# Performance work log

Measured on AMD Instinct MI355X. Metric: run time of the kernel, lower is better.

## Reference

```python
import jax, jax.numpy as jnp
import numpy as np

B, S, D, H = 2, 2048, 2048, 16
DK = D // H
EPS = 1e-5


def _layernorm(x, g, b):
    m = jnp.mean(x, axis=-1, keepdims=True)
    v = jnp.mean(jnp.square(x - m), axis=-1, keepdims=True)
    return (x - m) * jax.lax.rsqrt(v + EPS) * g + b


def setup_inputs() -> dict:
    key = jax.random.key(0)
    ks = jax.random.split(key, 12)
    w = lambda k, shape: jax.random.normal(k, shape, jnp.float32) * 0.02
    return {
        "src": jax.random.normal(ks[0], (B, S, D), jnp.float32),
        "src_mask": jnp.tril(jnp.ones((S, S), jnp.float32))[None, None],  # [1,1,S,S] causal
        "Wq": w(ks[1], (D, D)), "bq": jnp.zeros((D,), jnp.float32),
        "Wk": w(ks[2], (D, D)), "bk": jnp.zeros((D,), jnp.float32),
        "Wv": w(ks[3], (D, D)), "bv": jnp.zeros((D,), jnp.float32),
        "Wo": w(ks[4], (D, D)), "bo": jnp.zeros((D,), jnp.float32),
        "ln1_g": jnp.ones((D,), jnp.float32), "ln1_b": jnp.zeros((D,), jnp.float32),
        "ln2_g": jnp.ones((D,), jnp.float32), "ln2_b": jnp.zeros((D,), jnp.float32),
        "W1": w(ks[5], (D, 4 * D)), "b1": jnp.zeros((4 * D,), jnp.float32),
        "W2": w(ks[6], (4 * D, D)), "b2": jnp.zeros((D,), jnp.float32),
    }


def reference(src, src_mask, Wq, bq, Wk, bk, Wv, bv, Wo, bo,
              ln1_g, ln1_b, ln2_g, ln2_b, W1, b1, W2, b2):
    b, s, d = src.shape
    dk = d // H
    # --- pre-LN attention ---
    x = _layernorm(src, ln1_g, ln1_b)
    q = (x @ Wq + bq).reshape(b, s, H, dk).transpose(0, 2, 1, 3)  # [b,h,s,dk]
    k = (x @ Wk + bk).reshape(b, s, H, dk).transpose(0, 2, 1, 3)
    v = (x @ Wv + bv).reshape(b, s, H, dk).transpose(0, 2, 1, 3)
    scores = jnp.einsum('bhqd,bhkd->bhqk', q, k) / np.sqrt(dk).astype(np.float32)
    scores = jnp.where(src_mask > 0, scores, jnp.float32(-1e9))
    attn = jax.nn.softmax(scores, axis=-1)
    ctx = jnp.einsum('bhqk,bhkd->bhqd', attn, v)
    ctx = ctx.transpose(0, 2, 1, 3).reshape(b, s, d)
    x = src + (ctx @ Wo + bo)  # residual (dropout is identity at eval)
    # --- pre-LN MLP ---
    y = _layernorm(x, ln2_g, ln2_b)
    y = jax.nn.gelu(y @ W1 + b1, approximate=False) @ W2 + b2
    return x + y
```

## Files before the change

kernel.cpp:

```cpp
#include <hip/hip_runtime.h>
#include <hip/hip_bf16.h>
#include <math.h>

#define DEV __device__ __forceinline__

typedef __attribute__((ext_vector_type(8))) short short8;
typedef __attribute__((ext_vector_type(4))) float f32x4;

template<bool B> struct BoolC { static constexpr bool value = B; };

DEV short f2bf(float f) {
  union { float f; unsigned u; } v; v.f = f;
  unsigned r = v.u + 0x7fffu + ((v.u >> 16) & 1u);
  return (short)(r >> 16);
}

DEV void gload16(const void* g, void* l) {
  __builtin_amdgcn_global_load_lds(
      (__attribute__((address_space(1))) void*)g,
      (__attribute__((address_space(3))) void*)l, 16, 0, 0);
}

DEV void bar() {
  asm volatile("" ::: "memory");
  __builtin_amdgcn_s_barrier();
  asm volatile("" ::: "memory");
}
template<int N> DEV void vwait() {
  if constexpr (N == 0)      asm volatile("s_waitcnt vmcnt(0)" ::: "memory");
  else if constexpr (N == 3) asm volatile("s_waitcnt vmcnt(3)" ::: "memory");
  else                       asm volatile("s_waitcnt vmcnt(4)" ::: "memory");
}

__global__ __launch_bounds__(256) void ln_kernel(
    const float* __restrict__ x, const float* __restrict__ g,
    const float* __restrict__ b, short* __restrict__ out) {
  int row = blockIdx.x;
  const float* xr = x + (size_t)row * 2048;
  int tid = threadIdx.x;
  float4 a0 = ((const float4*)xr)[tid * 2];
  float4 a1 = ((const float4*)xr)[tid * 2 + 1];
  float s = a0.x + a0.y + a0.z + a0.w + a1.x + a1.y + a1.z + a1.w;
  float q = a0.x*a0.x + a0.y*a0.y + a0.z*a0.z + a0.w*a0.w
          + a1.x*a1.x + a1.y*a1.y + a1.z*a1.z + a1.w*a1.w;
#pragma unroll
  for (int off = 32; off; off >>= 1) { s += __shfl_xor(s, off); q += __shfl_xor(q, off); }
  __shared__ float red[8];
  int w = tid >> 6;
  if ((tid & 63) == 0) { red[w] = s; red[4 + w] = q; }
  __syncthreads();
  s = red[0] + red[1] + red[2] + red[3];
  q = red[4] + red[5] + red[6] + red[7];
  float mean = s * (1.0f / 2048.0f);
  float var  = q * (1.0f / 2048.0f) - mean * mean;
  float rstd = rsqrtf(var + 1e-5f);
  float xv[8] = {a0.x, a0.y, a0.z, a0.w, a1.x, a1.y, a1.z, a1.w};
  short8 o;
#pragma unroll
  for (int j = 0; j < 8; ++j) {
    int col = tid * 8 + j;
    o[j] = f2bf((xv[j] - mean) * rstd * g[col] + b[col]);
  }
  *(short8*)(out + (size_t)row * 2048 + tid * 8) = o;
}

__global__ __launch_bounds__(256) void wt_kernel(
    const float* __restrict__ W, short* __restrict__ Wt, int K, int N) {
  __shared__ short tile[64][65];
  int k0 = blockIdx.x * 64, n0 = blockIdx.y * 64;
  int tx = threadIdx.x, ty = threadIdx.y;
#pragma unroll
  for (int r = 0; r < 16; ++r) {
    int kl = ty + r * 4;
    tile[kl][tx] = f2bf(W[(size_t)(k0 + kl) * N + n0 + tx]);
  }
  __syncthreads();
#pragma unroll
  for (int r = 0; r < 16; ++r) {
    int nl = ty + r * 4;
    Wt[(size_t)(n0 + nl) * K + k0 + tx] = tile[tx][nl];
  }
}

template <int BM, int EPI>
__global__ __launch_bounds__(512, 2) void gemm8_kernel(
    const short* __restrict__ A, const short* __restrict__ Bt, int K, int N,
    const float* __restrict__ bp1, const float* __restrict__ bp2,
    const float* __restrict__ bp3, const float* __restrict__ res,
    short* __restrict__ outb, float* __restrict__ outf, short* __restrict__ vt) {
  constexpr int MF  = BM / 32;
  constexpr int MG  = MF / 2;
  constexpr int SA  = BM * 64;
  constexpr int SB  = 16384;
  constexpr int CPA = BM / 128;
  constexpr int CPB = 2;
  constexpr int NW  = CPA + CPB;
  __shared__ char lds[4 * SA + 4 * SB];
  char* Ab = lds;
  char* Bb = lds + 4 * SA;
  int tid = threadIdx.x, lane = tid & 63, w = tid >> 6;
  int wm = w >> 2, wn = w & 3, hi = lane >> 4, lo = lane & 15;
  int bm = blockIdx.y * BM, bn = blockIdx.x * 256;

  const char* gA[CPA]; int lA[CPA];
  const char* gB[CPB]; int lB[CPB];
#pragma unroll
  for (int i = 0; i < CPA; ++i) {
    int c = w * CPA + i, r = c * 16 + (lane >> 2);
    gA[i] = (const char*)(A + (size_t)(bm + r) * K) + (((lane & 3) ^ ((r >> 1) & 3)) << 4);
    lA[i] = c * 1024;
  }
#pragma unroll
  for (int i = 0; i < CPB; ++i) {
    int c = w * CPB + i, r = c * 16 + (lane >> 2);
    gB[i] = (const char*)(Bt + (size_t)(bn + r) * K) + (((lane & 3) ^ ((r >> 1) & 3)) << 4);
    lB[i] = c * 1024;
  }
  auto stA = [&](int g) {
    char* d = Ab + (g & 3) * SA;
#pragma unroll
    for (int i = 0; i < CPA; ++i) gload16(gA[i] + (size_t)g * 64, d + lA[i]);
  };
  auto stB = [&](int g) {
    char* d = Bb + (g & 3) * SB;
#pragma unroll
    for (int i = 0; i < CPB; ++i) gload16(gB[i] + (size_t)g * 64, d + lB[i]);
  };

  int offA[MF], offB[4];
#pragma unroll
  for (int m = 0; m < MF; ++m) {
    int r = wm * (BM / 2) + m * 16 + lo;
    offA[m] = r * 64 + ((hi ^ ((r >> 1) & 3)) << 4);
  }
#pragma unroll
  for (int n = 0; n < 4; ++n) {
    int r = wn * 64 + n * 16 + lo;
    offB[n] = r * 64 + ((hi ^ ((r >> 1) & 3)) << 4);
  }

  f32x4 acc[MF][4];
#pragma unroll
  for (int m = 0; m < MF; ++m)
#pragma unroll
    for (int n = 0; n < 4; ++n) acc[m][n] = (f32x4){0.f, 0.f, 0.f, 0.f};

  stA(0); stB(0); stA(1); stB(1);
  vwait<NW>(); bar();

  int NT = K >> 6;
  auto tile = [&](int t, auto stc) {
    constexpr bool ST = decltype(stc)::value;
    char* sa0 = Ab + ((2 * t) & 3) * SA;     char* sb0 = Bb + ((2 * t) & 3) * SB;
    char* sa1 = Ab + ((2 * t + 1) & 3) * SA; char* sb1 = Bb + ((2 * t + 1) & 3) * SB;
    short8 bf[4], af[MG];
#pragma unroll
    for (int n = 0; n < 4; ++n) bf[n] = *(const short8*)(sb0 + offB[n]);
#pragma unroll
    for (int m = 0; m < MG; ++m) af[m] = *(const short8*)(sa0 + offA[m]);
    if constexpr (ST) stA(2 * t + 2);
    bar(); __builtin_amdgcn_s_setprio(1);
#pragma unroll
    for (int m = 0; m < MG; ++m)
#pragma unroll
      for (int n = 0; n < 4; ++n)
        acc[m][n] = __builtin_amdgcn_mfma_f32_16x16x32_bf16(af[m], bf[n], acc[m][n], 0, 0, 0);
    __builtin_amdgcn_s_setprio(0); bar();
#pragma unroll
    for (int m = 0; m < MG; ++m) af[m] = *(const short8*)(sa0 + offA[MG + m]);
    if constexpr (ST) stB(2 * t + 2);
    bar(); __builtin_amdgcn_s_setprio(1);
#pragma unroll
    for (int m = 0; m < MG; ++m)
#pragma unroll
      for (int n = 0; n < 4; ++n)
        acc[MG + m][n] = __builtin_amdgcn_mfma_f32_16x16x32_bf16(af[m], bf[n], acc[MG + m][n], 0, 0, 0);
    __builtin_amdgcn_s_setprio(0);
    if constexpr (ST) vwait<NW>(); else vwait<0>();
    bar();
#pragma unroll
    for (int n = 0; n < 4; ++n) bf[n] = *(const short8*)(sb1 + offB[n]);
#pragma unroll
    for (int m = 0; m < MG; ++m) af[m] = *(const short8*)(sa1 + offA[m]);
    if constexpr (ST) stA(2 * t + 3);
    bar(); __builtin_amdgcn_s_setprio(1);
#pragma unroll
    for (int m = 0; m < MG; ++m)
#pragma unroll
      for (int n = 0; n < 4; ++n)
        acc[m][n] = __builtin_amdgcn_mfma_f32_16x16x32_bf16(af[m], bf[n], acc[m][n], 0, 0, 0);
    __builtin_amdgcn_s_setprio(0); bar();
#pragma unroll
    for (int m = 0; m < MG; ++m) af[m] = *(const short8*)(sa1 + offA[MG + m]);
    if constexpr (ST) stB(2 * t + 3);
    bar(); __builtin_amdgcn_s_setprio(1);
#pragma unroll
    for (int m = 0; m < MG; ++m)
#pragma unroll
      for (int n = 0; n < 4; ++n)
        acc[MG + m][n] = __builtin_amdgcn_mfma_f32_16x16x32_bf16(af[m], bf[n], acc[MG + m][n], 0, 0, 0);
    __builtin_amdgcn_s_setprio(0);
    if constexpr (ST) vwait<NW>();
    bar();
  };

  for (int t = 0; t < NT - 1; ++t) tile(t, BoolC<true>{});
  tile(NT - 1, BoolC<false>{});

#pragma unroll
  for (int mf = 0; mf < MF; ++mf) {
#pragma unroll
    for (int nf = 0; nf < 4; ++nf) {
      int n = bn + wn * 64 + nf * 16 + lo;
#pragma unroll
      for (int r = 0; r < 4; ++r) {
        int m = bm + wm * (BM / 2) + mf * 16 + hi * 4 + r;
        float v = acc[mf][nf][r];
        if (EPI == 0) {
          float bb = (n < 2048) ? bp1[n] : (n < 4096) ? bp2[n - 2048] : bp3[n - 4096];
          v += bb;
          if (n < 2048) v *= 0.08838834764831845f;
          outb[(size_t)m * N + n] = f2bf(v);
          if (n >= 4096) {
            int b_ = m >> 11, s_ = m & 2047, h_ = (n - 4096) >> 7, dk = (n - 4096) & 127;
            vt[((size_t)((b_ * 16 + h_) * 128 + dk) << 11) + s_] = f2bf(v);
          }
        } else if (EPI == 1) {
          outf[(size_t)m * N + n] = res[(size_t)m * N + n] + v + bp1[n];
        } else {
          float t = v + bp1[n];
          outb[(size_t)m * N + n] = f2bf(0.5f * t * (1.0f + erff(t * 0.70710678118654752f)));
        }
      }
    }
  }
}

__global__ __launch_bounds__(256) void attn_kernel(
    const short* __restrict__ qkv, const short* __restrict__ vtb,
    short* __restrict__ ctx) {
  __shared__ char Kl[16384];
  __shared__ char Vl[16384];
  __shared__ char Pl[16384];
  int qt = blockIdx.x, bh = blockIdx.y;
  int b = bh >> 4, h = bh & 15;
  int tid = threadIdx.x, lane = tid & 63, w = tid >> 6;
  int hi = lane >> 4, lo = lane & 15;

  short8 qf[2][4];
#pragma unroll
  for (int mi = 0; mi < 2; ++mi)
#pragma unroll
    for (int ks = 0; ks < 4; ++ks) {
      int row = b * 2048 + qt * 128 + w * 32 + mi * 16 + lo;
      int col = h * 128 + ks * 32 + hi * 8;
      qf[mi][ks] = *(const short8*)(qkv + (size_t)row * 6144 + col);
    }

  f32x4 ao[2][8] = {};
  float mst[2][4], lst[2][4];
#pragma unroll
  for (int i = 0; i < 2; ++i)
#pragma unroll
    for (int r = 0; r < 4; ++r) { mst[i][r] = -1e30f; lst[i][r] = 0.f; }

  int nt = 2 * qt + 2;
  for (int t = 0; t < nt; ++t) {
    __syncthreads();
#pragma unroll
    for (int i = 0; i < 4; ++i) {
      int c = w * 4 + i;
      int kr = c * 4 + (lane >> 4);
      int dk16 = lo ^ (kr & 7);
      const short* kg = qkv + (size_t)(b * 2048 + t * 64 + kr) * 6144
                            + 2048 + h * 128 + dk16 * 8;
      gload16(kg, Kl + c * 1024);
      int vr = c * 8 + (lane >> 3);
      int kv16 = (lane & 7) ^ (vr & 7);
      const short* vg = vtb + (size_t)(bh * 128 + vr) * 2048 + t * 64 + kv16 * 8;
      gload16(vg, Vl + c * 1024);
    }
    __syncthreads();

    f32x4 sc[2][4] = {};
#pragma unroll
    for (int ks = 0; ks < 4; ++ks) {
      short8 kf[4];
#pragma unroll
      for (int ni = 0; ni < 4; ++ni) {
        int r = ni * 16 + lo;
        kf[ni] = *(const short8*)(Kl + r * 256 + (((ks * 4 + hi) ^ (r & 7)) << 4));
      }
#pragma unroll
      for (int mi = 0; mi < 2; ++mi)
#pragma unroll
        for (int ni = 0; ni < 4; ++ni)
          sc[mi][ni] = __builtin_amdgcn_mfma_f32_16x16x32_bf16(qf[mi][ks], kf[ni], sc[mi][ni], 0, 0, 0);
    }

    if (t >= 2 * qt) {
#pragma unroll
      for (int mi = 0; mi < 2; ++mi)
#pragma unroll
        for (int ni = 0; ni < 4; ++ni)
#pragma unroll
          for (int r = 0; r < 4; ++r) {
            int qrow = qt * 128 + w * 32 + mi * 16 + hi * 4 + r;
            int kv = t * 64 + ni * 16 + lo;
            if (kv > qrow) sc[mi][ni][r] = -1e9f;
          }
    }

#pragma unroll
    for (int mi = 0; mi < 2; ++mi)
#pragma unroll
      for (int r = 0; r < 4; ++r) {
        float vm = fmaxf(fmaxf(sc[mi][0][r], sc[mi][1][r]),
                         fmaxf(sc[mi][2][r], sc[mi][3][r]));
#pragma unroll
        for (int off = 8; off; off >>= 1) vm = fmaxf(vm, __shfl_xor(vm, off));
        float mn = fmaxf(mst[mi][r], vm);
        float corr = __expf(mst[mi][r] - mn);
        float ps = 0.f;
#pragma unroll
        for (int ni = 0; ni < 4; ++ni) {
          float p = __expf(sc[mi][ni][r] - mn);
          sc[mi][ni][r] = p; ps += p;
        }
#pragma unroll
        for (int off = 8; off; off >>= 1) ps += __shfl_xor(ps, off);
        lst[mi][r] = lst[mi][r] * corr + ps;
        mst[mi][r] = mn;
#pragma unroll
        for (int ni = 0; ni < 8; ++ni) ao[mi][ni][r] *= corr;
      }

#pragma unroll
    for (int mi = 0; mi < 2; ++mi)
#pragma unroll
      for (int ni = 0; ni < 4; ++ni)
#pragma unroll
        for (int r = 0; r < 4; ++r) {
          int rl = w * 32 + mi * 16 + hi * 4 + r;
          int byte = (rl * 128 + (ni * 16 + lo) * 2) ^ ((rl & 7) << 4);
          *(short*)(Pl + byte) = f2bf(sc[mi][ni][r]);
        }

#pragma unroll
    for (int ks = 0; ks < 2; ++ks) {
      short8 pf[2];
#pragma unroll
      for (int mi = 0; mi < 2; ++mi) {
        int r = w * 32 + mi * 16 + lo;
        pf[mi] = *(const short8*)(Pl + r * 128 + (((ks * 4 + hi) ^ (r & 7)) << 4));
      }
#pragma unroll
      for (int ni = 0; ni < 8; ++ni) {
        int r = ni * 16 + lo;
        short8 vf = *(const short8*)(Vl + r * 128 + (((ks * 4 + hi) ^ (r & 7)) << 4));
#pragma unroll
        for (int mi = 0; mi < 2; ++mi)
          ao[mi][ni] = __builtin_amdgcn_mfma_f32_16x16x32_bf16(pf[mi], vf, ao[mi][ni], 0, 0, 0);
      }
    }
  }

#pragma unroll
  for (int mi = 0; mi < 2; ++mi)
#pragma unroll
    for (int r = 0; r < 4; ++r) {
      float inv = 1.0f / lst[mi][r];
      int m = b * 2048 + qt * 128 + w * 32 + mi * 16 + hi * 4 + r;
#pragma unroll
      for (int ni = 0; ni < 8; ++ni) {
        int col = h * 128 + ni * 16 + lo;
        ctx[(size_t)m * 2048 + col] = f2bf(ao[mi][ni][r] * inv);
      }
    }
}

extern "C" void kernel_launch(void* const* d_in, const int* in_sizes, int n_in,
                              void* d_out, int out_size, void* d_ws, size_t ws_size,
                              hipStream_t stream) {
  const float* src = (const float*)d_in[0];
  const float* Wq = (const float*)d_in[2];  const float* bq = (const float*)d_in[3];
  const float* Wk = (const float*)d_in[4];  const float* bk = (const float*)d_in[5];
  const float* Wv = (const float*)d_in[6];  const float* bv = (const float*)d_in[7];
  const float* Wo = (const float*)d_in[8];  const float* bo = (const float*)d_in[9];
  const float* g1 = (const float*)d_in[10]; const float* be1 = (const float*)d_in[11];
  const float* g2 = (const float*)d_in[12]; const float* be2 = (const float*)d_in[13];
  const float* W1 = (const float*)d_in[14]; const float* b1 = (const float*)d_in[15];
  const float* W2 = (const float*)d_in[16]; const float* b2 = (const float*)d_in[17];

  char* ws = (char*)d_ws;
  short* x_ln = (short*)(ws);
  short* qkvb = (short*)(ws + 16777216);
  short* vtb  = (short*)(ws + 67108864);
  short* ctxb = (short*)(ws + 83886080);
  float* xbuf = (float*)(ws + 100663296);
  short* wt   = (short*)(ws + 134217728);
  short* hb   = (short*)(ws + 16777216);

  dim3 tb(64, 4);

  wt_kernel<<<dim3(32, 32), tb, 0, stream>>>(Wq, wt,                2048, 2048);
  wt_kernel<<<dim3(32, 32), tb, 0, stream>>>(Wk, wt + 2048 * 2048,  2048, 2048);
  wt_kernel<<<dim3(32, 32), tb, 0, stream>>>(Wv, wt + 4096 * 2048,  2048, 2048);
  ln_kernel<<<4096, 256, 0, stream>>>(src, g1, be1, x_ln);
  gemm8_kernel<256, 0><<<dim3(24, 16), 512, 0, stream>>>(
      x_ln, wt, 2048, 6144, bq, bk, bv, nullptr, qkvb, nullptr, vtb);
  attn_kernel<<<dim3(16, 32), 256, 0, stream>>>(qkvb, vtb, ctxb);
  wt_kernel<<<dim3(32, 32), tb, 0, stream>>>(Wo, wt, 2048, 2048);
  gemm8_kernel<128, 1><<<dim3(8, 32), 512, 0, stream>>>(
      ctxb, wt, 2048, 2048, bo, nullptr, nullptr, src, nullptr, xbuf, nullptr);
  ln_kernel<<<4096, 256, 0, stream>>>(xbuf, g2, be2, x_ln);
  wt_kernel<<<dim3(32, 128), tb, 0, stream>>>(W1, wt, 2048, 8192);
  gemm8_kernel<256, 2><<<dim3(32, 16), 512, 0, stream>>>(
      x_ln, wt, 2048, 8192, b1, nullptr, nullptr, nullptr, hb, nullptr, nullptr);
  wt_kernel<<<dim3(128, 32), tb, 0, stream>>>(W2, wt, 8192, 2048);
  gemm8_kernel<128, 1><<<dim3(8, 32), 512, 0, stream>>>(
      hb, wt, 8192, 2048, b2, nullptr, nullptr, xbuf, nullptr, (float*)d_out, nullptr);

  (void)in_sizes; (void)n_in; (void)out_size; (void)ws_size;
}
```

Before: 985.7 us.

## Double-buffer K/V tiles and split attention across eight waves per block

The attention kernel moves from 4 waves owning 32 query rows each to 8 waves owning 16 rows, doubling threads per block. K and V tiles are double-buffered in LDS, so the next tile's global-to-LDS load is issued before computing on the current one, with a single wait and barrier per iteration. Waves whose query rows lie entirely before the KV tile now skip their compute, and the causal mask is applied only on diagonal tiles. LDS use grows to 80KB per block, which may limit how many blocks fit per CU.

```diff
diff --git a/kernel.cpp b/kernel.cpp
--- a/kernel.cpp
+++ b/kernel.cpp
@@ -236,147 +236,126 @@
   }
 }
 
-__global__ __launch_bounds__(256) void attn_kernel(
+__global__ __launch_bounds__(512, 4) void attn_kernel(
     const short* __restrict__ qkv, const short* __restrict__ vtb,
     short* __restrict__ ctx) {
-  __shared__ char Kl[16384];
-  __shared__ char Vl[16384];
+  __shared__ char Kl[2][16384];
+  __shared__ char Vl[2][16384];
   __shared__ char Pl[16384];
   int qt = blockIdx.x, bh = blockIdx.y;
   int b = bh >> 4, h = bh & 15;
   int tid = threadIdx.x, lane = tid & 63, w = tid >> 6;
   int hi = lane >> 4, lo = lane & 15;
-
-  short8 qf[2][4];
-#pragma unroll
-  for (int mi = 0; mi < 2; ++mi)
-#pragma unroll
-    for (int ks = 0; ks < 4; ++ks) {
-      int row = b * 2048 + qt * 128 + w * 32 + mi * 16 + lo;
-      int col = h * 128 + ks * 32 + hi * 8;
-      qf[mi][ks] = *(const short8*)(qkv + (size_t)row * 6144 + col);
+  int qrow0 = qt * 128 + w * 16;
+
+  short8 qf[4];
+#pragma unroll
+  for (int ks = 0; ks < 4; ++ks)
+    qf[ks] = *(const short8*)(qkv + (size_t)(b * 2048 + qrow0 + lo) * 6144
+                              + h * 128 + ks * 32 + hi * 8);
+
+  f32x4 ao[8] = {};
+  float mst[4], lst[4];
+#pragma unroll
+  for (int r = 0; r < 4; ++r) { mst[r] = -1e30f; lst[r] = 0.f; }
+
+  auto stage = [&](int t) {
+    int sl = t & 1;
+#pragma unroll
+    for (int i = 0; i < 2; ++i) {
+      int c = 2 * w + i;
+      int kr = c * 4 + (lane >> 4);
+      const short* kg = qkv + (size_t)(b * 2048 + t * 64 + kr) * 6144
+                            + 2048 + h * 128 + (lo ^ (kr & 7)) * 8;
+      gload16(kg, Kl[sl] + c * 1024);
+      int vr = c * 8 + (lane >> 3);
+      const short* vg = vtb + (size_t)(bh * 128 + vr) * 2048
+                            + t * 64 + ((lane & 7) ^ (vr & 7)) * 8;
+      gload16(vg, Vl[sl] + c * 1024);
     }
-
-  f32x4 ao[2][8] = {};
-  float mst[2][4], lst[2][4];
-#pragma unroll
-  for (int i = 0; i < 2; ++i)
-#pragma unroll
-    for (int r = 0; r < 4; ++r) { mst[i][r] = -1e30f; lst[i][r] = 0.f; }
+  };
+
+  stage(0);
+  vwait<0>(); bar();
 
   int nt = 2 * qt + 2;
   for (int t = 0; t < nt; ++t) {
-    __syncthreads();
-#pragma unroll
-    for (int i = 0; i < 4; ++i) {
-      int c = w * 4 + i;
-      int kr = c * 4 + (lane >> 4);
-      int dk16 = lo ^ (kr & 7);
-      const short* kg = qkv + (size_t)(b * 2048 + t * 64 + kr) * 6144
-                            + 2048 + h * 128 + dk16 * 8;
-      gload16(kg, Kl + c * 1024);
-      int vr = c * 8 + (lane >> 3);
-      int kv16 = (lane & 7) ^ (vr & 7);
-      const short* vg = vtb + (size_t)(bh * 128 + vr) * 2048 + t * 64 + kv16 * 8;
-      gload16(vg, Vl + c * 1024);
-    }
-    __syncthreads();
-
-    f32x4 sc[2][4] = {};
-#pragma unroll
-    for (int ks = 0; ks < 4; ++ks) {
-      short8 kf[4];
-#pragma unroll
-      for (int ni = 0; ni < 4; ++ni) {
-        int r = ni * 16 + lo;
-        kf[ni] = *(const short8*)(Kl + r * 256 + (((ks * 4 + hi) ^ (r & 7)) << 4));
+    if (t + 1 < nt) stage(t + 1);
+    const char* Ks = Kl[t & 1];
+    const char* Vs = Vl[t & 1];
+    int kv0 = t * 64;
+    if (kv0 <= qrow0 + 15) {
+      f32x4 sc[4] = {};
+#pragma unroll
+      for (int ks = 0; ks < 4; ++ks) {
+        short8 kf[4];
+#pragma unroll
+        for (int ni = 0; ni < 4; ++ni) {
+          int r = ni * 16 + lo;
+          kf[ni] = *(const short8*)(Ks + r * 256 + (((ks * 4 + hi) ^ (r & 7)) << 4));
+        }
+#pragma unroll
+        for (int ni = 0; ni < 4; ++ni)
+          sc[ni] = __builtin_amdgcn_mfma_f32_16x16x32_bf16(qf[ks], kf[ni], sc[ni], 0, 0, 0);
       }
-#pragma unroll
-      for (int mi = 0; mi < 2; ++mi)
+      if (kv0 + 63 > qrow0) {
 #pragma unroll
         for (int ni = 0; ni < 4; ++ni)
-          sc[mi][ni] = __builtin_amdgcn_mfma_f32_16x16x32_bf16(qf[mi][ks], kf[ni], sc[mi][ni], 0, 0, 0);
-    }
-
-    if (t >= 2 * qt) {
-#pragma unroll
-      for (int mi = 0; mi < 2; ++mi)
-#pragma unroll
-        for (int ni = 0; ni < 4; ++ni)
-#pragma unroll
-          for (int r = 0; r < 4; ++r) {
-            int qrow = qt * 128 + w * 32 + mi * 16 + hi * 4 + r;
-            int kv = t * 64 + ni * 16 + lo;
-            if (kv > qrow) sc[mi][ni][r] = -1e9f;
-          }
-    }
-
-#pragma unroll
-    for (int mi = 0; mi < 2; ++mi)
+#pragma unroll
+          for (int r = 0; r < 4; ++r)
+            if (kv0 + ni * 16 + lo > qrow0 + hi * 4 + r) sc[ni][r] = -1e9f;
+      }
 #pragma unroll
       for (int r = 0; r < 4; ++r) {
-        float vm = fmaxf(fmaxf(sc[mi][0][r], sc[mi][1][r]),
-                         fmaxf(sc[mi][2][r], sc[mi][3][r]));
+        float vm = fmaxf(fmaxf(sc[0][r], sc[1][r]), fmaxf(sc[2][r], sc[3][r]));
 #pragma unroll
         for (int off = 8; off; off >>= 1) vm = fmaxf(vm, __shfl_xor(vm, off));
-        float mn = fmaxf(mst[mi][r], vm);
-        float corr = __expf(mst[mi][r] - mn);
+        float mn = fmaxf(mst[r], vm);
+        float corr = __expf(mst[r] - mn);
         float ps = 0.f;
 #pragma unroll
         for (int ni = 0; ni < 4; ++ni) {
-          float p = __expf(sc[mi][ni][r] - mn);
-          sc[mi][ni][r] = p; ps += p;
+          float p = __expf(sc[ni][r] - mn);
+          sc[ni][r] = p; ps += p;
         }
 #pragma unroll
         for (int off = 8; off; off >>= 1) ps += __shfl_xor(ps, off);
-        lst[mi][r] = lst[mi][r] * corr + ps;
-        mst[mi][r] = mn;
-#pragma unroll
-        for (int ni = 0; ni < 8; ++ni) ao[mi][ni][r] *= corr;
+        lst[r] = lst[r] * corr + ps;
+        mst[r] = mn;
+#pragma unroll
+        for (int ni = 0; ni < 8; ++ni) ao[ni][r] *= corr;
       }
-
-#pragma unroll
-    for (int mi = 0; mi < 2; ++mi)
 #pragma unroll
       for (int ni = 0; ni < 4; ++ni)
 #pragma unroll
         for (int r = 0; r < 4; ++r) {
-          int rl = w * 32 + mi * 16 + hi * 4 + r;
+          int rl = hi * 4 + r;
           int byte = (rl * 128 + (ni * 16 + lo) * 2) ^ ((rl & 7) << 4);
-          *(short*)(Pl + byte) = f2bf(sc[mi][ni][r]);
+          *(short*)(Pl + w * 2048 + byte) = f2bf(sc[ni][r]);
         }
-
-#pragma unroll
-    for (int ks = 0; ks < 2; ++ks) {
-      short8 pf[2];
-#pragma unroll
-      for (int mi = 0; mi < 2; ++mi) {
-        int r = w * 32 + mi * 16 + lo;
-        pf[mi] = *(const short8*)(Pl + r * 128 + (((ks * 4 + hi) ^ (r & 7)) << 4));
-      }
-#pragma unroll
-      for (int ni = 0; ni < 8; ++ni) {
-        int r = ni * 16 + lo;
-        short8 vf = *(const short8*)(Vl + r * 128 + (((ks * 4 + hi) ^ (r & 7)) << 4));
-#pragma unroll
-        for (int mi = 0; mi < 2; ++mi)
-          ao[mi][ni] = __builtin_amdgcn_mfma_f32_16x16x32_bf16(pf[mi], vf, ao[mi][ni], 0, 0, 0);
+#pragma unroll
+      for (int ks = 0; ks < 2; ++ks) {
+        short8 pf = *(const short8*)(Pl + w * 2048 + lo * 128
+                                     + (((ks * 4 + hi) ^ (lo & 7)) << 4));
+#pragma unroll
+        for (int ni = 0; ni < 8; ++ni) {
+          int r = ni * 16 + lo;
+          short8 vf = *(const short8*)(Vs + r * 128 + (((ks * 4 + hi) ^ (r & 7)) << 4));
+          ao[ni] = __builtin_amdgcn_mfma_f32_16x16x32_bf16(pf, vf, ao[ni], 0, 0, 0);
+        }
       }
     }
-  }
-
-#pragma unroll
-  for (int mi = 0; mi < 2; ++mi)
-#pragma unroll
-    for (int r = 0; r < 4; ++r) {
-      float inv = 1.0f / lst[mi][r];
-      int m = b * 2048 + qt * 128 + w * 32 + mi * 16 + hi * 4 + r;
-#pragma unroll
-      for (int ni = 0; ni < 8; ++ni) {
-        int col = h * 128 + ni * 16 + lo;
-        ctx[(size_t)m * 2048 + col] = f2bf(ao[mi][ni][r] * inv);
-      }
-    }
+    vwait<0>(); bar();
+  }
+
+#pragma unroll
+  for (int r = 0; r < 4; ++r) {
+    float inv = 1.0f / lst[r];
+    int m = b * 2048 + qrow0 + hi * 4 + r;
+#pragma unroll
+    for (int ni = 0; ni < 8; ++ni)
+      ctx[(size_t)m * 2048 + h * 128 + ni * 16 + lo] = f2bf(ao[ni][r] * inv);
+  }
 }
 
 extern "C" void kernel_launch(void* const* d_in, const int* in_sizes, int n_in,
@@ -409,7 +388,7 @@
   ln_kernel<<<4096, 256, 0, stream>>>(src, g1, be1, x_ln);
   gemm8_kernel<256, 0><<<dim3(24, 16), 512, 0, stream>>>(
       x_ln, wt, 2048, 6144, bq, bk, bv, nullptr, qkvb, nullptr, vtb);
-  attn_kernel<<<dim3(16, 32), 256, 0, stream>>>(qkvb, vtb, ctxb);
+  attn_kernel<<<dim3(16, 32), 512, 0, stream>>>(qkvb, vtb, ctxb);
   wt_kernel<<<dim3(32, 32), tb, 0, stream>>>(Wo, wt, 2048, 2048);
   gemm8_kernel<128, 1><<<dim3(8, 32), 512, 0, stream>>>(
       ctxb, wt, 2048, 2048, bo, nullptr, nullptr, src, nullptr, xbuf, nullptr);
```

Result: faster. 920.6 us (-6.6%).
